# Kernel optimization log

Measured on AMD Instinct MI355X. Metric: run time of the kernel, lower is better.

The kernel has to match this reference:

```python
import jax, jax.numpy as jnp
import numpy as np

HIDDEN = 64
EMBED = 256

def gelu(x):
    # torch nn.GELU default = exact (erf) gelu
    return jax.nn.gelu(x, approximate=False)

def setup_inputs() -> dict:
    key = jax.random.key(0)
    ks = jax.random.split(key, 12)
    B, N, M, P, E, H = 4, 256, 512, 2, EMBED, HIDDEN
    def lin(k, fan_in, shape):
        bound = 1.0 / np.sqrt(fan_in)
        return jax.random.uniform(k, shape, jnp.float32, -bound, bound)
    return {
        "z": jax.random.uniform(ks[0], (M, P), jnp.float32),
        "mu": jax.random.uniform(ks[1], (B, N, P), jnp.float32),
        "embeddings": jax.random.normal(ks[2], (B, N, E), jnp.float32),
        # FiLM generator: Linear(E,H) -> GELU -> Linear(H,2H)
        "fg_w1": lin(ks[3], E, (H, E)), "fg_b1": lin(ks[4], E, (H,)),
        "fg_w2": lin(ks[5], H, (2 * H, H)), "fg_b2": lin(ks[6], H, (2 * H,)),
        # kernel net: Linear(1,H), Linear(H,H), Linear(H,1)
        "kn_w0": lin(ks[7], 1, (H, 1)), "kn_b0": lin(ks[8], 1, (H,)),
        "kn_w2": lin(ks[9], H, (H, H)), "kn_b2": lin(ks[10], H, (H,)),
        "kn_w4": lin(ks[11], H, (1, H)), "kn_b4": lin(jax.random.fold_in(key, 99), H, (1,)),
    }

def reference(z, mu, embeddings, fg_w1, fg_b1, fg_w2, fg_b2,
              kn_w0, kn_b0, kn_w2, kn_b2, kn_w4, kn_b4):
    # pairwise distances [B, N, M]
    diff = z[None, None, :, :] - mu[:, :, None, :]
    distances = jnp.linalg.norm(diff, axis=-1)
    nd = distances / (jnp.max(distances) + 1e-8)
    # FiLM params from embeddings: [B, N, H] each
    h = gelu(jnp.einsum('bne,he->bnh', embeddings, fg_w1) + fg_b1)
    film = jnp.einsum('bnh,gh->bng', h, fg_w2) + fg_b2
    H = kn_b0.shape[0]
    scale = film[..., :H][:, :, None, :]   # [B, N, 1, H]
    shift = film[..., H:][:, :, None, :]
    # kernel net with FiLM modulation, broadcast over grid dim M
    x = nd[..., None] * kn_w0[:, 0] + kn_b0        # Linear(1,H) -> [B, N, M, H]
    x = gelu(scale * x + shift)
    x = jnp.einsum('bnmh,gh->bnmg', x, kn_w2) + kn_b2
    x = gelu(scale * x + shift)
    x = jnp.einsum('bnmh,gh->bnmg', x, kn_w4) + kn_b4  # [B, N, M, 1]
    return jax.nn.sigmoid(x[..., 0])               # [B, N, M]
```

## Files before the change

### kernel.cpp

```cpp
#include <hip/hip_runtime.h>
#include <hip/hip_bf16.h>
#include <math.h>

#define B_ 4
#define N_ 256
#define M_ 512
#define E_ 256
#define H_ 64

typedef __attribute__((ext_vector_type(8))) short bf16x8;
typedef __attribute__((ext_vector_type(4))) float f32x4;
typedef __attribute__((ext_vector_type(2))) float f32x2;

__device__ __forceinline__ f32x2 pfma(f32x2 a, f32x2 b, f32x2 c) {
    return __builtin_elementwise_fma(a, b, c);
}

__device__ __forceinline__ f32x2 gelu2(f32x2 x) {
    f32x2 t = x * x;
    f32x2 k2; k2.x = -0.10294377f; k2.y = -0.10294377f;
    f32x2 k1; k1.x = -2.3022081f;  k1.y = -2.3022081f;
    f32x2 u = pfma(t, k2, k1);
    f32x2 un = x * u;
    f32x2 E;
    E.x = __builtin_amdgcn_exp2f(un.x);
    E.y = __builtin_amdgcn_exp2f(un.y);
    f32x2 one; one.x = 1.0f; one.y = 1.0f;
    f32x2 d = E + one;
    f32x2 r; r.x = __builtin_amdgcn_rcpf(d.x); r.y = __builtin_amdgcn_rcpf(d.y);
    return x * r;
}

__device__ __forceinline__ float gelu_e(float x) {
    return 0.5f * x * (1.0f + erff(x * 0.70710678118654752f));
}

__device__ __forceinline__ short sbf(float f) {
    __bf16 h = (__bf16)f;
    return __builtin_bit_cast(short, h);
}

__global__ __launch_bounds__(256) void film_params_kernel(
    const float* __restrict__ z, const float* __restrict__ mu,
    const float* __restrict__ emb,
    const float* __restrict__ fg_w1, const float* __restrict__ fg_b1,
    const float* __restrict__ fg_w2, const float* __restrict__ fg_b2,
    const float* __restrict__ kn_w0, const float* __restrict__ kn_b0,
    const float* __restrict__ kn_b2,
    unsigned* __restrict__ wsmax, float* __restrict__ pmax,
    float* __restrict__ par, int sb) {
    __shared__ float s_emb[E_];
    __shared__ float s_part[256];
    __shared__ float s_h[H_];
    __shared__ float s_sc[H_], s_sh[H_];
    __shared__ float s_mx[4];
    const int t = threadIdx.x;
    const int bn = blockIdx.x;

    s_emb[t] = emb[bn * E_ + t];

    float mu0 = mu[2 * bn], mu1 = mu[2 * bn + 1];
    float2 z0 = ((const float2*)z)[t];
    float2 z1 = ((const float2*)z)[t + 256];
    float d0 = z0.x - mu0, d1 = z0.y - mu1;
    float mx = fmaf(d0, d0, d1 * d1);
    d0 = z1.x - mu0; d1 = z1.y - mu1;
    mx = fmaxf(mx, fmaf(d0, d0, d1 * d1));
    #pragma unroll
    for (int off = 32; off; off >>= 1) mx = fmaxf(mx, __shfl_xor(mx, off, 64));
    if ((t & 63) == 0) s_mx[t >> 6] = mx;
    __syncthreads();
    if (t == 0) {
        float m4 = fmaxf(fmaxf(s_mx[0], s_mx[1]), fmaxf(s_mx[2], s_mx[3]));
        if (pmax) pmax[bn] = m4;
        else atomicMax(wsmax, __float_as_uint(m4));
    }

    {
        int h = t & 63, q = t >> 6;
        const f32x2* wr = (const f32x2*)(fg_w1 + h * E_ + q * 64);
        const f32x2* er = (const f32x2*)(s_emb + q * 64);
        f32x2 a2; a2.x = 0.f; a2.y = 0.f;
        #pragma unroll
        for (int e = 0; e < 32; e++) a2 = pfma(wr[e], er[e], a2);
        s_part[t] = a2.x + a2.y;
    }
    __syncthreads();
    if (t < H_) {
        float hv = s_part[t] + s_part[64 + t] + s_part[128 + t] + s_part[192 + t] + fg_b1[t];
        s_h[t] = gelu_e(hv);
    }
    __syncthreads();
    {
        int g = t >> 1, hf = t & 1;
        const f32x2* wr = (const f32x2*)(fg_w2 + g * H_ + hf * 32);
        const f32x2* hr = (const f32x2*)(s_h + hf * 32);
        f32x2 a2; a2.x = 0.f; a2.y = 0.f;
        #pragma unroll
        for (int q2 = 0; q2 < 16; q2++) a2 = pfma(wr[q2], hr[q2], a2);
        float acc = a2.x + a2.y;
        acc += __shfl_xor(acc, 1, 64);
        if (!hf) {
            float val = acc + fg_b2[g];
            if (g < H_) s_sc[g] = val; else s_sh[g - H_] = val;
        }
    }
    __syncthreads();
    if (t < H_) {
        float sc = s_sc[t], sh = s_sh[t];
        float* p0 = par + bn * sb;
        p0[t]          = sc * kn_w0[t];
        p0[H_ + t]     = fmaf(sc, kn_b0[t], sh);
        p0[2 * H_ + t] = fmaf(sc, kn_b2[t], sh);
        p0[3 * H_ + t] = sc;
    }
}

__global__ __launch_bounds__(512, 4) void film_main_kernel(
    const float* __restrict__ z, const float* __restrict__ mu,
    const float* __restrict__ kn_w2, const float* __restrict__ kn_w4,
    const float* __restrict__ kn_b4,
    const unsigned* __restrict__ wsmax, const float* __restrict__ pmax,
    const float* __restrict__ par, int sb,
    float* __restrict__ out) {
    __shared__ __align__(16) float s_T[H_];
    __shared__ __align__(16) float s_w4[H_];
    __shared__ bf16x8 s_bfr[8][64];
    __shared__ float s_mx[4];
    const int t = threadIdx.x;
    const int bn = blockIdx.x;
    const int lane = t & 63, wid = t >> 6;
    const int kg = lane >> 4, cl = lane & 15;
    const int mbase = wid * 64;

    const float* pb = par + bn * sb;

    float2 zz[4];
    #pragma unroll
    for (int tl = 0; tl < 4; tl++) zz[tl] = ((const float2*)z)[mbase + tl * 16 + cl];

    f32x4 A1v[2][2], A0v[2][2];
    #pragma unroll
    for (int c = 0; c < 2; c++)
        #pragma unroll
        for (int q = 0; q < 2; q++) {
            A1v[c][q] = *(const f32x4*)(pb + c * 32 + kg * 8 + q * 4);
            A0v[c][q] = *(const f32x4*)(pb + 64 + c * 32 + kg * 8 + q * 4);
        }

    if (t < 64) s_T[t] = pb[128 + t];
    else if (t < 128) s_w4[t - 64] = kn_w4[t - 64];

    if (pmax) {
        if (t < 256) {
            f32x4 pv = ((const f32x4*)pmax)[t];
            float mym = fmaxf(fmaxf(pv[0], pv[1]), fmaxf(pv[2], pv[3]));
            #pragma unroll
            for (int off = 32; off; off >>= 1) mym = fmaxf(mym, __shfl_xor(mym, off, 64));
            if (lane == 0) s_mx[wid] = mym;
        }
    }

    {
        int c = wid >> 2, ct = wid & 3;
        float Sg = pb[192 + ct * 16 + cl];
        const float* wr = kn_w2 + (ct * 16 + cl) * H_ + c * 32 + kg * 8;
        f32x4 w0v = *(const f32x4*)(wr);
        f32x4 w1v = *(const f32x4*)(wr + 4);
        bf16x8 v;
        #pragma unroll
        for (int i = 0; i < 4; i++) {
            v[i]     = sbf(w0v[i] * Sg);
            v[4 + i] = sbf(w1v[i] * Sg);
        }
        s_bfr[wid][lane] = v;
    }

    float mu0 = mu[bn * 2], mu1 = mu[bn * 2 + 1];
    float b4v = kn_b4[0];

    __syncthreads();
    float maxd2 = pmax
        ? fmaxf(fmaxf(s_mx[0], s_mx[1]), fmaxf(s_mx[2], s_mx[3]))
        : __uint_as_float(*wsmax);
    float invd = __builtin_amdgcn_rcpf(__builtin_amdgcn_sqrtf(maxd2) + 1e-8f);
    float* outr = out + bn * M_ + mbase;

    #pragma unroll
    for (int tl = 0; tl < 4; ++tl) {
        float dz0 = zz[tl].x - mu0, dz1 = zz[tl].y - mu1;
        float nd = __builtin_amdgcn_sqrtf(fmaf(dz0, dz0, dz1 * dz1)) * invd;
        f32x2 ndv; ndv.x = nd; ndv.y = nd;

        bf16x8 xf[2];
        #pragma unroll
        for (int c = 0; c < 2; c++) {
            bf16x8 v;
            #pragma unroll
            for (int q = 0; q < 2; q++) {
                f32x2 x1a; x1a.x = A1v[c][q][0]; x1a.y = A1v[c][q][1];
                f32x2 x1b; x1b.x = A1v[c][q][2]; x1b.y = A1v[c][q][3];
                f32x2 x0a; x0a.x = A0v[c][q][0]; x0a.y = A0v[c][q][1];
                f32x2 x0b; x0b.x = A0v[c][q][2]; x0b.y = A0v[c][q][3];
                f32x2 g1 = gelu2(pfma(ndv, x1a, x0a));
                f32x2 g2 = gelu2(pfma(ndv, x1b, x0b));
                v[q * 4]     = sbf(g1.x); v[q * 4 + 1] = sbf(g1.y);
                v[q * 4 + 2] = sbf(g2.x); v[q * 4 + 3] = sbf(g2.y);
            }
            xf[c] = v;
        }

        f32x2 y2; y2.x = 0.f; y2.y = 0.f;
        #pragma unroll
        for (int ct = 0; ct < 4; ct++) {
            f32x4 a = *(const f32x4*)(s_T + ct * 16 + kg * 4);
            a = __builtin_amdgcn_mfma_f32_16x16x32_bf16(s_bfr[ct][lane], xf[0], a, 0, 0, 0);
            a = __builtin_amdgcn_mfma_f32_16x16x32_bf16(s_bfr[4 + ct][lane], xf[1], a, 0, 0, 0);
            f32x4 wv = *(const f32x4*)(s_w4 + ct * 16 + kg * 4);
            f32x2 a01; a01.x = a[0]; a01.y = a[1];
            f32x2 a23; a23.x = a[2]; a23.y = a[3];
            f32x2 w01; w01.x = wv[0]; w01.y = wv[1];
            f32x2 w23; w23.x = wv[2]; w23.y = wv[3];
            y2 = pfma(gelu2(a01), w01, y2);
            y2 = pfma(gelu2(a23), w23, y2);
        }
        float y = y2.x + y2.y;
        y += __shfl_xor(y, 16, 64);
        y += __shfl_xor(y, 32, 64);

        if (kg == tl) {
            float E = __builtin_amdgcn_exp2f((y + b4v) * -1.44269504f);
            outr[tl * 16 + cl] = __builtin_amdgcn_rcpf(1.0f + E);
        }
    }
}

extern "C" void kernel_launch(void* const* d_in, const int* in_sizes, int n_in,
                              void* d_out, int out_size, void* d_ws, size_t ws_size,
                              hipStream_t stream) {
    const float* z      = (const float*)d_in[0];
    const float* mu     = (const float*)d_in[1];
    const float* emb    = (const float*)d_in[2];
    const float* fg_w1  = (const float*)d_in[3];
    const float* fg_b1  = (const float*)d_in[4];
    const float* fg_w2  = (const float*)d_in[5];
    const float* fg_b2  = (const float*)d_in[6];
    const float* kn_w0  = (const float*)d_in[7];
    const float* kn_b0  = (const float*)d_in[8];
    const float* kn_w2  = (const float*)d_in[9];
    const float* kn_b2  = (const float*)d_in[10];
    const float* kn_w4  = (const float*)d_in[11];
    const float* kn_b4  = (const float*)d_in[12];
    float* out = (float*)d_out;

    const size_t need = 16384 + (size_t)(B_ * N_) * 256 * sizeof(float);
    if (ws_size >= need) {
        float* pmax = (float*)d_ws;
        float* par  = (float*)((char*)d_ws + 16384);
        film_params_kernel<<<B_ * N_, 256, 0, stream>>>(
            z, mu, emb, fg_w1, fg_b1, fg_w2, fg_b2, kn_w0, kn_b0, kn_b2,
            nullptr, pmax, par, 256);
        film_main_kernel<<<B_ * N_, 512, 0, stream>>>(
            z, mu, kn_w2, kn_w4, kn_b4, nullptr, pmax, par, 256, out);
    } else {
        unsigned* wsmax = (unsigned*)d_ws;
        float* par = out;
        hipMemsetAsync(d_ws, 0, 4, stream);
        film_params_kernel<<<B_ * N_, 256, 0, stream>>>(
            z, mu, emb, fg_w1, fg_b1, fg_w2, fg_b2, kn_w0, kn_b0, kn_b2,
            wsmax, nullptr, par, 512);
        film_main_kernel<<<B_ * N_, 512, 0, stream>>>(
            z, mu, kn_w2, kn_w4, kn_b4, wsmax, nullptr, par, 512, out);
    }
}
```

Before: 39.37 us.

## Compute final projection with MFMA and keep bias/w4 in registers

The final H->1 projection now runs on two extra bf16 MFMAs instead of per-lane FMAs plus cross-lane shuffles. The hidden-row order of the second layer is permuted so the MFMA output layout feeds straight into the next MFMA's B operand. The bias/shift vector T and the w4 weights are now held in registers instead of read from shared memory, removing LDS traffic and two shuffles per tile. The cost is extra bf16 rounding of the second GELU outputs and of w4, which lowers accuracy, plus more register pressure.

After: 39.25 us. Within noise of the previous version (-0.3%).

```diff
diff --git a/kernel.cpp b/kernel.cpp
--- a/kernel.cpp
+++ b/kernel.cpp
@@ -123,8 +123,6 @@
     const unsigned* __restrict__ wsmax, const float* __restrict__ pmax,
     const float* __restrict__ par, int sb,
     float* __restrict__ out) {
-    __shared__ __align__(16) float s_T[H_];
-    __shared__ __align__(16) float s_w4[H_];
     __shared__ bf16x8 s_bfr[8][64];
     __shared__ float s_mx[4];
     const int t = threadIdx.x;
@@ -148,8 +146,21 @@
             A0v[c][q] = *(const f32x4*)(pb + 64 + c * 32 + kg * 8 + q * 4);
         }
 
-    if (t < 64) s_T[t] = pb[128 + t];
-    else if (t < 128) s_w4[t - 64] = kn_w4[t - 64];
+    f32x4 Tr[4];
+    #pragma unroll
+    for (int ct = 0; ct < 4; ct++)
+        Tr[ct] = *(const f32x4*)(pb + 128 + (ct & 1) * 32 + kg * 8 + (ct >> 1) * 4);
+
+    bf16x8 wf[2];
+    #pragma unroll
+    for (int c = 0; c < 2; c++) {
+        f32x4 wa = *(const f32x4*)(kn_w4 + c * 32 + kg * 8);
+        f32x4 wb = *(const f32x4*)(kn_w4 + c * 32 + kg * 8 + 4);
+        bf16x8 v;
+        #pragma unroll
+        for (int i = 0; i < 4; i++) { v[i] = sbf(wa[i]); v[4 + i] = sbf(wb[i]); }
+        wf[c] = v;
+    }
 
     if (pmax) {
         if (t < 256) {
@@ -163,8 +174,9 @@
 
     {
         int c = wid >> 2, ct = wid & 3;
-        float Sg = pb[192 + ct * 16 + cl];
-        const float* wr = kn_w2 + (ct * 16 + cl) * H_ + c * 32 + kg * 8;
+        int row_g = (ct & 1) * 32 + (cl >> 2) * 8 + (ct >> 1) * 4 + (cl & 3);
+        float Sg = pb[192 + row_g];
+        const float* wr = kn_w2 + row_g * H_ + c * 32 + kg * 8;
         f32x4 w0v = *(const f32x4*)(wr);
         f32x4 w1v = *(const f32x4*)(wr + 4);
         bf16x8 v;
@@ -173,7 +185,7 @@
             v[i]     = sbf(w0v[i] * Sg);
             v[4 + i] = sbf(w1v[i] * Sg);
         }
-        s_bfr[wid][lane] = v;
+        s_bfr[c * 4 + ct][lane] = v;
     }
 
     float mu0 = mu[bn * 2], mu1 = mu[bn * 2 + 1];
@@ -210,26 +222,33 @@
             xf[c] = v;
         }
 
-        f32x2 y2; y2.x = 0.f; y2.y = 0.f;
+        f32x4 g4[4];
         #pragma unroll
         for (int ct = 0; ct < 4; ct++) {
-            f32x4 a = *(const f32x4*)(s_T + ct * 16 + kg * 4);
+            f32x4 a = Tr[ct];
             a = __builtin_amdgcn_mfma_f32_16x16x32_bf16(s_bfr[ct][lane], xf[0], a, 0, 0, 0);
             a = __builtin_amdgcn_mfma_f32_16x16x32_bf16(s_bfr[4 + ct][lane], xf[1], a, 0, 0, 0);
-            f32x4 wv = *(const f32x4*)(s_w4 + ct * 16 + kg * 4);
             f32x2 a01; a01.x = a[0]; a01.y = a[1];
             f32x2 a23; a23.x = a[2]; a23.y = a[3];
-            f32x2 w01; w01.x = wv[0]; w01.y = wv[1];
-            f32x2 w23; w23.x = wv[2]; w23.y = wv[3];
-            y2 = pfma(gelu2(a01), w01, y2);
-            y2 = pfma(gelu2(a23), w23, y2);
-        }
-        float y = y2.x + y2.y;
-        y += __shfl_xor(y, 16, 64);
-        y += __shfl_xor(y, 32, 64);
+            f32x2 g01 = gelu2(a01), g23 = gelu2(a23);
+            g4[ct][0] = g01.x; g4[ct][1] = g01.y; g4[ct][2] = g23.x; g4[ct][3] = g23.y;
+        }
+
+        bf16x8 pf0, pf1;
+        #pragma unroll
+        for (int i = 0; i < 4; i++) {
+            pf0[i]     = sbf(g4[0][i]);
+            pf0[4 + i] = sbf(g4[2][i]);
+            pf1[i]     = sbf(g4[1][i]);
+            pf1[4 + i] = sbf(g4[3][i]);
+        }
+
+        f32x4 yb; yb[0] = b4v; yb[1] = b4v; yb[2] = b4v; yb[3] = b4v;
+        yb = __builtin_amdgcn_mfma_f32_16x16x32_bf16(wf[0], pf0, yb, 0, 0, 0);
+        yb = __builtin_amdgcn_mfma_f32_16x16x32_bf16(wf[1], pf1, yb, 0, 0, 0);
 
         if (kg == tl) {
-            float E = __builtin_amdgcn_exp2f((y + b4v) * -1.44269504f);
+            float E = __builtin_amdgcn_exp2f(yb[0] * -1.44269504f);
             outr[tl * 16 + cl] = __builtin_amdgcn_rcpf(1.0f + E);
         }
     }
```
